# Optimization experiments

Hardware: AMD Instinct MI355X
Metric: run time of the kernel (lower is better)

## Reference

```python
import jax, jax.numpy as jnp
import numpy as np

B, C, H, W = 8, 256, 64, 64
HEADS, PTS = 8, 4
HD = C // HEADS
CIN_G, CIN_S, COUT = 1024, 320, 320


def _sine_pe(c, h, w):
    # LoFTR-style 2D sinusoidal position encoding, returns [C,H,W]
    pe = np.zeros((c, h, w), dtype=np.float32)
    y = np.broadcast_to(np.arange(h, dtype=np.float32)[None, :, None], (1, h, w))
    x = np.broadcast_to(np.arange(w, dtype=np.float32)[None, None, :], (1, h, w))
    div = np.exp(np.arange(0, c // 2, 2, dtype=np.float32) * (-np.log(10000.0) / (c // 2)))[:, None, None]
    pe[0::4] = np.sin(x * div)
    pe[1::4] = np.cos(x * div)
    pe[2::4] = np.sin(y * div)
    pe[3::4] = np.cos(y * div)
    return jnp.asarray(pe)


def _ref_points(h, w):
    # faithful to source: meshgrid over (W,H) 'ij', stack (col,row), flatten w-major
    rows = np.linspace(0, 1, w, dtype=np.float32)
    cols = np.linspace(0, 1, h, dtype=np.float32)
    R, Cg = np.meshgrid(rows, cols, indexing='ij')  # [W,H]
    return jnp.asarray(np.stack([Cg, R], -1).reshape(-1, 2))  # [W*H,2]


PE = _sine_pe(C, H, W)
RP = _ref_points(H, W)


def conv1x1(x, w, b):
    return jnp.einsum('bchw,oc->bohw', x, w) + b[None, :, None, None]


def deform_attn(qf, vf, vp_w, vp_b, so_w, so_b, aw_w, aw_b, op_w, op_b):
    # qf: [B,Nq,C]  vf: [B,Nv,C]  (single level, H x W value map)
    Bn, Nq, Cc = qf.shape
    v = (vf @ vp_w + vp_b).reshape(Bn, -1, HEADS, HD).transpose(0, 2, 1, 3)  # [B,h,Nv,hd]
    off = (qf @ so_w + so_b).reshape(Bn, Nq, HEADS, PTS, 2)
    aw = jax.nn.softmax((qf @ aw_w + aw_b).reshape(Bn, Nq, HEADS, PTS), axis=-1)
    loc = RP[None, :, None, None, :] + off / jnp.array([W, H], qf.dtype)  # [B,Nq,h,P,2]
    # grid_sample align_corners=False, zero padding
    px = loc[..., 0] * W - 0.5
    py = loc[..., 1] * H - 0.5
    x0 = jnp.floor(px).astype(jnp.int32)
    y0 = jnp.floor(py).astype(jnp.int32)
    wx = px - x0
    wy = py - y0
    out = jnp.zeros((Bn, HEADS, Nq, PTS, HD), qf.dtype)
    for dx, dy, wgt in ((0, 0, (1 - wx) * (1 - wy)), (1, 0, wx * (1 - wy)),
                        (0, 1, (1 - wx) * wy), (1, 1, wx * wy)):
        xi = x0 + dx
        yi = y0 + dy
        valid = ((xi >= 0) & (xi < W) & (yi >= 0) & (yi < H)).astype(qf.dtype)
        idx = jnp.clip(yi, 0, H - 1) * W + jnp.clip(xi, 0, W - 1)  # [B,Nq,h,P]
        idx_h = idx.transpose(0, 2, 1, 3).reshape(Bn, HEADS, Nq * PTS)
        g = jnp.take_along_axis(v, idx_h[..., None], axis=2).reshape(Bn, HEADS, Nq, PTS, HD)
        out = out + g * (wgt * valid).transpose(0, 2, 1, 3)[..., None]
    o = (out * aw.transpose(0, 2, 1, 3)[..., None]).sum(3)  # [B,h,Nq,hd]
    o = o.transpose(0, 2, 1, 3).reshape(Bn, Nq, Cc)
    return o @ op_w + op_b + qf  # mmcv: output_proj + identity (dropout=eval)


def cross_attn(q, value, vp_w, vp_b, so_w, so_b, aw_w, aw_b, op_w, op_b):
    qp = q + PE[None]  # query += pe
    qf = qp.reshape(qp.shape[0], C, H * W).transpose(0, 2, 1)
    vf = value.reshape(value.shape[0], C, H * W).transpose(0, 2, 1)
    o = deform_attn(qf, vf, vp_w, vp_b, so_w, so_b, aw_w, aw_b, op_w, op_b)
    o = o.transpose(0, 2, 1).reshape(qp.shape)
    return o + qp


def setup_inputs() -> dict:
    key = jax.random.key(0)
    ks = jax.random.split(key, 40)
    inp = {}
    inp['ground'] = jax.random.normal(ks[0], (B, CIN_G, H, W), jnp.float32)
    inp['sat'] = jax.random.normal(ks[1], (B, CIN_S, H, W), jnp.float32)
    inp['osm'] = jax.random.normal(ks[2], (B, CIN_S, H, W), jnp.float32)
    i = [3]
    def p(name, shape, scale=0.02):
        inp[name] = jax.random.normal(ks[i[0]], shape, jnp.float32) * scale
        i[0] += 1
    p('gc_w', (C, CIN_G)); p('gc_b', (C,))
    p('sc_w', (C, CIN_S)); p('sc_b', (C,))
    p('up_w', (COUT, C)); p('up_b', (COUT,))
    p('a_w1', (C, 64)); p('a_b1', (64,))
    p('a_w2', (64, 1)); p('a_b2', (1,))
    for pre in ('sat_', 'osm_'):
        p(pre + 'vp_w', (C, C)); p(pre + 'vp_b', (C,))
        p(pre + 'so_w', (C, HEADS * PTS * 2)); p(pre + 'so_b', (HEADS * PTS * 2,))
        p(pre + 'aw_w', (C, HEADS * PTS)); p(pre + 'aw_b', (HEADS * PTS,))
        p(pre + 'op_w', (C, C)); p(pre + 'op_b', (C,))
    inp['index'] = 0
    return inp


def reference(ground, sat, osm, gc_w, gc_b, sc_w, sc_b, up_w, up_b,
              a_w1, a_b1, a_w2, a_b2,
              sat_vp_w, sat_vp_b, sat_so_w, sat_so_b, sat_aw_w, sat_aw_b, sat_op_w, sat_op_b,
              osm_vp_w, osm_vp_b, osm_so_w, osm_so_b, osm_aw_w, osm_aw_b, osm_op_w, osm_op_b,
              index):
    del index  # params for index=0 already selected
    g = conv1x1(ground, gc_w, gc_b)
    s = conv1x1(sat, sc_w, sc_b)
    o = conv1x1(osm, sc_w, sc_b)  # source bug: osm projected with sat_convs
    gf = g.reshape(B, C, H * W).transpose(0, 2, 1)
    alpha = jax.nn.sigmoid(jax.nn.relu(gf @ a_w1 + a_b1) @ a_w2 + a_b2)  # [B,Nq,1]
    a = alpha.mean(axis=1)[:, :, None, None]  # [B,1,1,1]
    sat_out = cross_attn(g, s, sat_vp_w, sat_vp_b, sat_so_w, sat_so_b, sat_aw_w, sat_aw_b, sat_op_w, sat_op_b)
    # torch in-place `query += pe` inside ca_sat mutates `ground`, so ca_osm sees g + PE
    osm_out = cross_attn(g + PE[None], o, osm_vp_w, osm_vp_b, osm_so_w, osm_so_b, osm_aw_w, osm_aw_b, osm_op_w, osm_op_b)
    fused = a * sat_out + (1.0 - a) * osm_out
    return conv1x1(fused, up_w, up_b), a
```

## Files before the change

kernel.cpp:

```cpp
#include <hip/hip_runtime.h>
#include <cstddef>
#include <cstdint>

#define NB 8
#define NQ 4096

typedef __attribute__((ext_vector_type(8))) short bfrag8;
typedef __attribute__((ext_vector_type(4))) float facc4;
typedef __attribute__((ext_vector_type(4))) unsigned short us4;
typedef __attribute__((ext_vector_type(8))) unsigned short us8;

__device__ __forceinline__ float bf2f(unsigned short u) {
  union { unsigned int i; float f; } v; v.i = ((unsigned int)u) << 16; return v.f;
}
__device__ __forceinline__ unsigned short f2bf(float f) {
  union { float f; unsigned int i; } v; v.f = f;
  unsigned int r = v.i + 0x7FFFu + ((v.i >> 16) & 1u);
  return (unsigned short)(r >> 16);
}
__device__ __forceinline__ void gload16(const void* g, void* l) {
  __builtin_amdgcn_global_load_lds(
      (const __attribute__((address_space(1))) void*)g,
      (__attribute__((address_space(3))) void*)l, 16, 0, 0);
}

struct PrepArgs {
  const float *gc_w, *up_w, *up_b;
  const float *so_w0, *so_b0, *so_w1, *so_b1;
  const float *aw_w0, *aw_b0, *aw_w1, *aw_b1;
  const float *a_w1;
  const float *op_w0, *op_w1;
  unsigned short *PET, *WG, *WUP, *OPT0, *OPT1, *SOWS;
  float *BUPP, *SOBS;
};

__global__ __launch_bounds__(256) void mega_prep(PrepArgs p) {
  const int blk = blockIdx.x, t = threadIdx.x;
  if (blk < 4096) {
    int idx = blk * 256 + t;
    int q = idx >> 8, c = idx & 255;
    int h = q >> 6, w = q & 63;
    int k = c >> 2, m = c & 3;
    float dv = expf((float)(2 * k) * (-9.210340371976184f / 128.0f));
    float arg = ((m < 2) ? (float)w : (float)h) * dv;
    p.PET[idx] = f2bf(((m & 1) == 0) ? sinf(arg) : cosf(arg));
  } else if (blk < 5120) {
    int i = (blk - 4096) * 256 + t;
    p.WG[i] = f2bf(p.gc_w[i]);
  } else if (blk < 5504) {
    int i = (blk - 5120) * 256 + t;
    int m = i >> 8, k = i & 255;
    p.WUP[i] = (m < 320) ? f2bf(p.up_w[m * 256 + k]) : 0;
  } else if (blk < 5505) {
    p.BUPP[t] = (t < 320) ? p.up_b[t] : 0.f;
    if (t < 128) {
      int i2 = 256 + t;
      p.BUPP[i2] = (i2 < 320) ? p.up_b[i2] : 0.f;
    }
  } else if (blk < 6017) {
    int i = (blk - 5505) * 256 + t;
    int which = i >> 16, j = i & 65535;
    int o = j >> 8, k = j & 255;
    (which ? p.OPT1 : p.OPT0)[j] = f2bf((which ? p.op_w1 : p.op_w0)[k * 256 + o]);
  } else {
    int i = (blk - 6017) * 256 + t;
    int row = i >> 8, k = i & 255;
    float v = 0.f;
    if (row < 256) {
      int br = row >> 7, rr = row & 127;
      const float* sw = br ? p.so_w1 : p.so_w0;
      const float* aw = br ? p.aw_w1 : p.aw_w0;
      if (rr < 64) v = sw[k * 64 + rr];
      else if (rr < 96) v = aw[k * 32 + (rr - 64)];
    } else if (row < 320) {
      v = p.a_w1[k * 64 + (row - 256)];
    }
    p.SOWS[i] = f2bf(v);
    if (i < 256) {
      int br = i >> 7, rr = i & 127;
      const float* sb = br ? p.so_b1 : p.so_b0;
      const float* ab = br ? p.aw_b1 : p.aw_b0;
      p.SOBS[i] = (rr < 64) ? sb[rr] : ((rr < 96) ? ab[rr - 64] : 0.f);
    }
  }
}

__global__ __launch_bounds__(256) void k_wv(const float* __restrict__ vp_w0,
                                            const float* __restrict__ vp_b0,
                                            const float* __restrict__ vp_w1,
                                            const float* __restrict__ vp_b1,
                                            const float* __restrict__ sc_w,
                                            const float* __restrict__ sc_b,
                                            unsigned short* __restrict__ WV0,
                                            unsigned short* __restrict__ WV1,
                                            float* __restrict__ BV0,
                                            float* __restrict__ BV1) {
  const int br = blockIdx.y, kt = blockIdx.x, k0 = kt * 20, t = threadIdx.x;
  const float* vp = br ? vp_w1 : vp_w0;
  unsigned short* WV = br ? WV1 : WV0;
  __shared__ float vt[32][256];
  __shared__ float st[32][20];
  __shared__ float sb[32];
  float acc[20] = {};
  float accB = 0.f;
  for (int c0 = 0; c0 < 256; c0 += 32) {
    __syncthreads();
#pragma unroll
    for (int cc = 0; cc < 32; ++cc)
      vt[cc][t] = vp[(size_t)(c0 + cc) * 256 + t];
    for (int i = t; i < 640; i += 256)
      st[i / 20][i % 20] = sc_w[(size_t)(c0 + i / 20) * 320 + k0 + (i % 20)];
    if (t < 32) sb[t] = sc_b[c0 + t];
    __syncthreads();
#pragma unroll
    for (int cc = 0; cc < 32; ++cc) {
      float v = vt[cc][t];
      accB = fmaf(v, sb[cc], accB);
#pragma unroll
      for (int j = 0; j < 20; ++j)
        acc[j] = fmaf(v, st[cc][j], acc[j]);
    }
  }
#pragma unroll
  for (int j = 0; j < 20; ++j) WV[(size_t)t * 320 + k0 + j] = f2bf(acc[j]);
  if (kt == 0) (br ? BV1 : BV0)[t] = (br ? vp_b1 : vp_b0)[t] + accB;
}

struct GArgs {
  const unsigned short* W[2];
  const unsigned short* X[2];
  const float* bias[2];
  void* out[2];
  float rscale[2];
  int K, ldm, bmask, brshift;
};
template <int MODE>
__global__ __launch_bounds__(256) void gemm_bf16(GArgs g) {
  __shared__ unsigned short As[8192];
  __shared__ unsigned short Bs[8192];
  const int t = threadIdx.x;
  const int lane = t & 63, w = t >> 6;
  const int z = blockIdx.z;
  const int b = z & g.bmask, br = z >> g.brshift;
  const int K = g.K;
  const int n0 = blockIdx.x * 128;
  const unsigned short* W = g.W[br];
  const unsigned short* Xb = g.X[br] + (size_t)b * NQ * K;

  const unsigned short* asrc[4];
  const unsigned short* bsrc[4];
  unsigned short* adst[4];
  unsigned short* bdst[4];
#pragma unroll
  for (int i = 0; i < 4; ++i) {
    int cid = i * 256 + t;
    int row = cid >> 3;
    int cc = (cid & 7) ^ (row & 7);
    asrc[i] = W + (size_t)row * K + cc * 8;
    bsrc[i] = Xb + (size_t)(n0 + row) * K + cc * 8;
    adst[i] = &As[i * 2048 + w * 512];
    bdst[i] = &Bs[i * 2048 + w * 512];
  }
  const int wm = (w >> 1) * 64, wn = (w & 1) * 64;
  const int l15 = lane & 15, l4 = lane >> 4;
  facc4 acc[4][4];
#pragma unroll
  for (int i = 0; i < 4; ++i)
#pragma unroll
    for (int j = 0; j < 4; ++j) acc[i][j] = facc4{0.f, 0.f, 0.f, 0.f};

  for (int k0 = 0; k0 < K; k0 += 64) {
    if (k0) __syncthreads();
#pragma unroll
    for (int i = 0; i < 4; ++i) {
      gload16(asrc[i], adst[i]);
      gload16(bsrc[i], bdst[i]);
      asrc[i] += 64; bsrc[i] += 64;
    }
    __syncthreads();
#pragma unroll
    for (int kk = 0; kk < 2; ++kk) {
      bfrag8 af[4], bf[4];
#pragma unroll
      for (int mi = 0; mi < 4; ++mi) {
        int row = wm + mi * 16 + l15;
        af[mi] = *reinterpret_cast<const bfrag8*>(&As[row * 64 + (((kk * 4 + l4) ^ (row & 7)) * 8)]);
      }
#pragma unroll
      for (int ni = 0; ni < 4; ++ni) {
        int row = wn + ni * 16 + l15;
        bf[ni] = *reinterpret_cast<const bfrag8*>(&Bs[row * 64 + (((kk * 4 + l4) ^ (row & 7)) * 8)]);
      }
#pragma unroll
      for (int mi = 0; mi < 4; ++mi)
#pragma unroll
        for (int ni = 0; ni < 4; ++ni)
          acc[mi][ni] = __builtin_amdgcn_mfma_f32_16x16x32_bf16(af[mi], bf[ni], acc[mi][ni], 0, 0, 0);
    }
  }
  const size_t bq = (size_t)b * NQ;
#pragma unroll
  for (int mi = 0; mi < 4; ++mi) {
#pragma unroll
    for (int ni = 0; ni < 4; ++ni) {
      int m = wm + mi * 16 + l4 * 4;
      int n = n0 + wn + ni * 16 + l15;
      facc4 v = acc[mi][ni];
      unsigned short* o16 = (unsigned short*)g.out[br];
      float sc = g.rscale[br];
      float4 bv = *reinterpret_cast<const float4*>(&g.bias[br][m]);
      us4 pk;
      pk[0] = f2bf(v[0] * sc + bv.x); pk[1] = f2bf(v[1] * sc + bv.y);
      pk[2] = f2bf(v[2] * sc + bv.z); pk[3] = f2bf(v[3] * sc + bv.w);
      *reinterpret_cast<us4*>(&o16[(bq + n) * g.ldm + m]) = pk;
    }
  }
}

struct NArgs {
  const unsigned short* W[2];
  const void* X[2];
  const float* bias[2];
  void* out[2];
  const unsigned short* G;
  const unsigned short* PET;
  const float* afin;
  float rs[2];
  int K, zmask, zshift;
};
template <int BSRC, int MODE>
__global__ __launch_bounds__(256) void gemm_n64(NArgs g) {
  __shared__ unsigned short As[16384];
  __shared__ unsigned short Bs[4096];
  const int t = threadIdx.x;
  const int lane = t & 63, w = t >> 6;
  const int z = blockIdx.z;
  const int b = z & g.zmask, br = z >> g.zshift;
  const int K = g.K;
  const int n0 = blockIdx.x * 64;

  const unsigned short* W = g.W[br];
  const unsigned short* asrc[8];
  unsigned short* adst[8];
#pragma unroll
  for (int i = 0; i < 8; ++i) {
    int c = t + 256 * i;
    int row = c >> 3;
    int k8 = (c & 7) ^ (row & 7);
    asrc[i] = W + (size_t)row * K + k8 * 8;
    adst[i] = &As[w * 512 + i * 2048];
  }

  const unsigned short* bsrc16[2];
  unsigned short* bdst16[2];
  const float* bsrcf = nullptr;
  const int kb = t >> 4, nb = t & 15;
  if constexpr (BSRC == 0) {
    const unsigned short* Xh = (const unsigned short*)g.X[br];
#pragma unroll
    for (int i = 0; i < 2; ++i) {
      int c = t + 256 * i;
      int n = c >> 3;
      int k8 = (c & 7) ^ (n & 7);
      bsrc16[i] = Xh + ((size_t)b * NQ + n0 + n) * K + k8 * 8;
      bdst16[i] = &Bs[w * 512 + i * 2048];
    }
  } else {
    const float* Xf = (const float*)g.X[br];
    bsrcf = Xf + (size_t)b * K * NQ + (size_t)(kb * 4) * NQ + n0 + nb * 4;
  }

  const int l15 = lane & 15, l4 = lane >> 4;
  facc4 acc[4][4];
#pragma unroll
  for (int i = 0; i < 4; ++i)
#pragma unroll
    for (int j = 0; j < 4; ++j) acc[i][j] = facc4{0.f, 0.f, 0.f, 0.f};

  for (int k0 = 0; k0 < K; k0 += 64) {
    if (k0) __syncthreads();
#pragma unroll
    for (int i = 0; i < 8; ++i) {
      gload16(asrc[i], adst[i]);
      asrc[i] += 64;
    }
    if constexpr (BSRC == 0) {
      gload16(bsrc16[0], bdst16[0]); bsrc16[0] += 64;
      gload16(bsrc16[1], bdst16[1]); bsrc16[1] += 64;
    } else {
      float vv[4][4];
#pragma unroll
      for (int r = 0; r < 4; ++r) {
        float4 v = *reinterpret_cast<const float4*>(bsrcf + (size_t)k0 * NQ + (size_t)r * NQ);
        vv[r][0] = v.x; vv[r][1] = v.y; vv[r][2] = v.z; vv[r][3] = v.w;
      }
#pragma unroll
      for (int c = 0; c < 4; ++c) {
        int n = nb * 4 + c;
        us4 pk;
        pk[0] = f2bf(vv[0][c]); pk[1] = f2bf(vv[1][c]);
        pk[2] = f2bf(vv[2][c]); pk[3] = f2bf(vv[3][c]);
        int off = n * 64 + (((kb >> 1) ^ (n & 7)) * 8) + (kb & 1) * 4;
        *reinterpret_cast<us4*>(&Bs[off]) = pk;
      }
    }
    __syncthreads();
#pragma unroll
    for (int kk = 0; kk < 2; ++kk) {
      bfrag8 af[4], bf[4];
#pragma unroll
      for (int mi = 0; mi < 4; ++mi) {
        int row = w * 64 + mi * 16 + l15;
        af[mi] = *reinterpret_cast<const bfrag8*>(&As[row * 64 + (((kk * 4 + l4) ^ (row & 7)) * 8)]);
      }
#pragma unroll
      for (int ni = 0; ni < 4; ++ni) {
        int row = ni * 16 + l15;
        bf[ni] = *reinterpret_cast<const bfrag8*>(&Bs[row * 64 + (((kk * 4 + l4) ^ (row & 7)) * 8)]);
      }
#pragma unroll
      for (int mi = 0; mi < 4; ++mi)
#pragma unroll
        for (int ni = 0; ni < 4; ++ni)
          acc[mi][ni] = __builtin_amdgcn_mfma_f32_16x16x32_bf16(af[mi], bf[ni], acc[mi][ni], 0, 0, 0);
    }
  }

  const size_t bq = (size_t)b * NQ;
  unsigned short* o16 = (unsigned short*)g.out[br];
#pragma unroll
  for (int mi = 0; mi < 4; ++mi) {
#pragma unroll
    for (int ni = 0; ni < 4; ++ni) {
      int m = w * 64 + mi * 16 + l4 * 4;
      int n = n0 + ni * 16 + l15;
      facc4 v = acc[mi][ni];
      float4 bv = *reinterpret_cast<const float4*>(&g.bias[br][m]);
      float rv[4] = {v[0] + bv.x, v[1] + bv.y, v[2] + bv.z, v[3] + bv.w};
      if constexpr (MODE == 6) {
        float a = g.afin[b];
        float s = br ? (1.f - a) : a;
        float rsc = g.rs[br];
        us4 gv = *reinterpret_cast<const us4*>(&g.G[(bq + n) * 256 + m]);
        us4 pv = *reinterpret_cast<const us4*>(&g.PET[(size_t)n * 256 + m]);
#pragma unroll
        for (int r = 0; r < 4; ++r)
          rv[r] = s * (rv[r] + 2.f * bf2f(gv[r]) + rsc * bf2f(pv[r]));
      }
      us4 pk;
#pragma unroll
      for (int r = 0; r < 4; ++r) pk[r] = f2bf(rv[r]);
      *reinterpret_cast<us4*>(&o16[(bq + n) * 256 + m]) = pk;
    }
  }
}

struct SAArgs {
  const unsigned short *W;
  const unsigned short *G;
  const unsigned short *PESOS;
  const float *b1, *w2, *b2;
  unsigned short *SWS;
  float *partial;
};
__global__ __launch_bounds__(384) void k_swalpha(SAArgs g) {
  __shared__ unsigned short As[24576];
  __shared__ unsigned short Bs[4096];
  const int t = threadIdx.x;
  const int lane = t & 63, w = t >> 6;
  const int b = blockIdx.z;
  const int n0 = blockIdx.x * 64;

  const unsigned short* asrc[8];
  unsigned short* adst[8];
#pragma unroll
  for (int i = 0; i < 8; ++i) {
    int c = t + 384 * i;
    int row = c >> 3;
    int k8 = (c & 7) ^ (row & 7);
    asrc[i] = g.W + (size_t)row * 256 + k8 * 8;
    adst[i] = &As[w * 512 + i * 3072];
  }
  const bool bst = t < 256;
  const unsigned short* bsrc[2];
// ... 60 lines not shown
        int m = w * 64 + mi * 16 + l4 * 4;
        int n = n0 + ni * 16 + l15;
        facc4 v = acc[mi][ni];
        us4 rr = *reinterpret_cast<const us4*>(&g.PESOS[(size_t)n * 256 + m]);
        us4 pk;
#pragma unroll
        for (int r = 0; r < 4; ++r) pk[r] = f2bf(v[r] + bf2f(rr[r]));
        *reinterpret_cast<us4*>(&g.SWS[(bq + n) * 256 + m]) = pk;
      }
    }
  } else if (w == 4) {
    float b2v = g.b2[0];
    float ssum = 0.f;
#pragma unroll
    for (int ni = 0; ni < 4; ++ni) {
      float s = 0.f;
#pragma unroll
      for (int mi = 0; mi < 4; ++mi) {
#pragma unroll
        for (int r = 0; r < 4; ++r) {
          int hid = mi * 16 + l4 * 4 + r;
          s += fmaxf(acc[mi][ni][r] + g.b1[hid], 0.f) * g.w2[hid];
        }
      }
      s += __shfl_xor(s, 16);
      s += __shfl_xor(s, 32);
      ssum += 1.f / (1.f + expf(-(s + b2v)));
    }
    ssum += __shfl_xor(ssum, 1);
    ssum += __shfl_xor(ssum, 2);
    ssum += __shfl_xor(ssum, 4);
    ssum += __shfl_xor(ssum, 8);
    if (lane == 0) g.partial[b * 64 + blockIdx.x] = ssum;
  }
}

__global__ __launch_bounds__(64) void k_alpha_fin(const float* __restrict__ partial,
                                                  float* __restrict__ afin,
                                                  float* __restrict__ out_a) {
  int b = blockIdx.x;
  float s = partial[b * 64 + threadIdx.x];
#pragma unroll
  for (int off = 32; off; off >>= 1) s += __shfl_xor(s, off);
  if (threadIdx.x == 0) {
    float a = s * (1.f / 4096.f);
    afin[b] = a;
    out_a[b] = a;
  }
}

__global__ __launch_bounds__(384) void gemm_up(const unsigned short* __restrict__ W,
                                               const unsigned short* __restrict__ S0,
                                               const unsigned short* __restrict__ S1,
                                               const float* __restrict__ bias,
                                               float* __restrict__ out) {
  __shared__ unsigned short As[24576];
  __shared__ unsigned short Bs[4096];
  const int t = threadIdx.x;
  const int lane = t & 63, w = t >> 6;
  const int b = blockIdx.z;
  const int n0 = blockIdx.x * 64;

  const unsigned short* asrc[8];
  unsigned short* adst[8];
#pragma unroll
  for (int i = 0; i < 8; ++i) {
    int c = t + 384 * i;
    int row = c >> 3;
    int k8 = (c & 7) ^ (row & 7);
    asrc[i] = W + (size_t)row * 256 + k8 * 8;
    adst[i] = &As[w * 512 + i * 3072];
  }
  const bool bst = t < 256;
  size_t bidx[2];
  if (bst) {
#pragma unroll
    for (int i = 0; i < 2; ++i) {
      int c = t + 256 * i;
      int n = c >> 3;
      int bk8 = (c & 7) ^ (n & 7);
      bidx[i] = ((size_t)b * NQ + n0 + n) * 256 + bk8 * 8;
    }
  }

  const int l15 = lane & 15, l4 = lane >> 4;
  facc4 acc[4][4];
#pragma unroll
  for (int i = 0; i < 4; ++i)
#pragma unroll
    for (int j = 0; j < 4; ++j) acc[i][j] = facc4{0.f, 0.f, 0.f, 0.f};

  for (int k0 = 0; k0 < 256; k0 += 64) {
    if (k0) __syncthreads();
#pragma unroll
    for (int i = 0; i < 8; ++i) {
      gload16(asrc[i], adst[i]);
      asrc[i] += 64;
    }
    if (bst) {
#pragma unroll
      for (int i = 0; i < 2; ++i) {
        us8 x = *reinterpret_cast<const us8*>(&S0[bidx[i] + k0]);
        us8 y = *reinterpret_cast<const us8*>(&S1[bidx[i] + k0]);
        us8 o;
#pragma unroll
        for (int j = 0; j < 8; ++j) o[j] = f2bf(bf2f(x[j]) + bf2f(y[j]));
        *reinterpret_cast<us8*>(&Bs[(t + 256 * i) * 8]) = o;
      }
    }
    __syncthreads();
#pragma unroll
    for (int kk = 0; kk < 2; ++kk) {
      bfrag8 af[4], bf[4];
#pragma unroll
      for (int mi = 0; mi < 4; ++mi) {
        int row = w * 64 + mi * 16 + l15;
        af[mi] = *reinterpret_cast<const bfrag8*>(&As[row * 64 + (((kk * 4 + l4) ^ (row & 7)) * 8)]);
      }
#pragma unroll
      for (int ni = 0; ni < 4; ++ni) {
        int row = ni * 16 + l15;
        bf[ni] = *reinterpret_cast<const bfrag8*>(&Bs[row * 64 + (((kk * 4 + l4) ^ (row & 7)) * 8)]);
      }
#pragma unroll
      for (int mi = 0; mi < 4; ++mi)
#pragma unroll
        for (int ni = 0; ni < 4; ++ni)
          acc[mi][ni] = __builtin_amdgcn_mfma_f32_16x16x32_bf16(af[mi], bf[ni], acc[mi][ni], 0, 0, 0);
    }
  }
#pragma unroll
  for (int mi = 0; mi < 4; ++mi) {
    int m = w * 64 + mi * 16 + l4 * 4;
    if (m >= 320) continue;
#pragma unroll
    for (int ni = 0; ni < 4; ++ni) {
      int n = n0 + ni * 16 + l15;
      facc4 v = acc[mi][ni];
#pragma unroll
      for (int r = 0; r < 4; ++r)
        out[((size_t)b * 320 + m + r) * NQ + n] = v[r] + bias[m + r];
    }
  }
}

__global__ __launch_bounds__(256) void k_sample(const unsigned short* __restrict__ VP0,
                                                const unsigned short* __restrict__ VP1,
                                                const unsigned short* __restrict__ SWS,
                                                unsigned short* __restrict__ OATT0,
                                                unsigned short* __restrict__ OATT1) {
  int y = blockIdx.y;
  int b = y & 7, br = y >> 3;
  int q0 = blockIdx.x * 8;
  const unsigned short* VP = (br ? VP1 : VP0) + (size_t)b * NQ * 256;
  const unsigned short* SWp = SWS + ((size_t)b * NQ + q0) * 256 + br * 128;
  unsigned short* OATT = (br ? OATT1 : OATT0) + ((size_t)b * NQ + q0) * 256;
  __shared__ unsigned short sws[1024];
  int t = threadIdx.x;
  {
    int row = t >> 5, col = (t & 31) * 4;
    *reinterpret_cast<us4*>(&sws[row * 128 + col]) =
        *reinterpret_cast<const us4*>(&SWp[(size_t)row * 256 + col]);
  }
  __syncthreads();
  int qi = t >> 5, ss = t & 31, head = ss >> 2, hdg = ss & 3;
  int q = q0 + qi;
  const unsigned short* sw = &sws[qi * 128];
  float l0 = bf2f(sw[64 + head * 4 + 0]);
  float l1 = bf2f(sw[64 + head * 4 + 1]);
  float l2 = bf2f(sw[64 + head * 4 + 2]);
  float l3 = bf2f(sw[64 + head * 4 + 3]);
  float mx = fmaxf(fmaxf(l0, l1), fmaxf(l2, l3));
  float e0 = expf(l0 - mx), e1 = expf(l1 - mx), e2 = expf(l2 - mx), e3 = expf(l3 - mx);
  float inv = 1.f / (e0 + e1 + e2 + e3);
  float aw[4] = {e0 * inv, e1 * inv, e2 * inv, e3 * inv};
  float rpx = (float)(q & 63) * (64.f / 63.f) - 0.5f;
  float rpy = (float)(q >> 6) * (64.f / 63.f) - 0.5f;
  const unsigned short* vb = VP + head * 32 + hdg * 8;
  float acc[8] = {};
#pragma unroll
  for (int p = 0; p < 4; ++p) {
    float px = rpx + bf2f(sw[head * 8 + p * 2 + 0]);
    float py = rpy + bf2f(sw[head * 8 + p * 2 + 1]);
    float fx = floorf(px), fy = floorf(py);
    int x0 = (int)fx, y0 = (int)fy;
    float wx = px - fx, wy = py - fy;
#pragma unroll
    for (int dy = 0; dy < 2; ++dy) {
#pragma unroll
      for (int dx = 0; dx < 2; ++dx) {
        int xi = x0 + dx, yi = y0 + dy;
        if (xi >= 0 && xi < 64 && yi >= 0 && yi < 64) {
          float wa = aw[p] * (dx ? wx : 1.f - wx) * (dy ? wy : 1.f - wy);
          bfrag8 v = *reinterpret_cast<const bfrag8*>(&vb[(size_t)(yi * 64 + xi) * 256]);
#pragma unroll
          for (int j = 0; j < 8; ++j) acc[j] = fmaf(wa, bf2f((unsigned short)v[j]), acc[j]);
        }
      }
    }
  }
  us8 o;
#pragma unroll
  for (int j = 0; j < 8; ++j) o[j] = f2bf(acc[j]);
  *reinterpret_cast<us8*>(&OATT[qi * 256 + ss * 8]) = o;
}

extern "C" void kernel_launch(void* const* d_in, const int* in_sizes, int n_in,
                              void* d_out, int out_size, void* d_ws, size_t ws_size,
                              hipStream_t stream) {
  const float* ground = (const float*)d_in[0];
  const float* sat = (const float*)d_in[1];
  const float* osm = (const float*)d_in[2];
  const float* gc_w = (const float*)d_in[3];
  const float* gc_b = (const float*)d_in[4];
  const float* sc_w = (const float*)d_in[5];
  const float* sc_b = (const float*)d_in[6];
  const float* up_w = (const float*)d_in[7];
  const float* up_b = (const float*)d_in[8];
  const float* a_w1 = (const float*)d_in[9];
  const float* a_b1 = (const float*)d_in[10];
  const float* a_w2 = (const float*)d_in[11];
  const float* a_b2 = (const float*)d_in[12];
  const float* vp_w[2] = {(const float*)d_in[13], (const float*)d_in[21]};
  const float* vp_b[2] = {(const float*)d_in[14], (const float*)d_in[22]};
  const float* so_w[2] = {(const float*)d_in[15], (const float*)d_in[23]};
  const float* so_b[2] = {(const float*)d_in[16], (const float*)d_in[24]};
  const float* aw_w[2] = {(const float*)d_in[17], (const float*)d_in[25]};
  const float* aw_b[2] = {(const float*)d_in[18], (const float*)d_in[26]};
  const float* op_w[2] = {(const float*)d_in[19], (const float*)d_in[27]};
  const float* op_b[2] = {(const float*)d_in[20], (const float*)d_in[28]};

  char* wsb = (char*)d_ws;
  const size_t MBy = 1 << 20;
  unsigned short* PET  = (unsigned short*)(wsb);
  unsigned short* WG   = (unsigned short*)(wsb + 2 * MBy);
  unsigned short* WV0  = (unsigned short*)(wsb + 2 * MBy + 524288);
  unsigned short* WV1  = (unsigned short*)(wsb + 2 * MBy + 786432);
  unsigned short* WUP  = (unsigned short*)(wsb + 3 * MBy);
  unsigned short* OPT0 = (unsigned short*)(wsb + 3 * MBy + 262144);
  unsigned short* OPT1 = (unsigned short*)(wsb + 3 * MBy + 393216);
  unsigned short* SOWS = (unsigned short*)(wsb + 3 * MBy + 524288);
  unsigned short* PESOS = (unsigned short*)(wsb + 4 * MBy);
  float* SOBS = (float*)(wsb + 6 * MBy);
  float* BV0  = (float*)(wsb + 6 * MBy + 4096);
  float* BV1  = (float*)(wsb + 6 * MBy + 8192);
  float* BUPP = (float*)(wsb + 6 * MBy + 12288);
  float* PART = (float*)(wsb + 6 * MBy + 16384);
  float* AFIN = (float*)(wsb + 6 * MBy + 32768);
  unsigned short* G     = (unsigned short*)(wsb + 8 * MBy);
  unsigned short* VP0b  = (unsigned short*)(wsb + 24 * MBy);
  unsigned short* VP1b  = (unsigned short*)(wsb + 40 * MBy);
  unsigned short* SWS   = (unsigned short*)(wsb + 56 * MBy);
  unsigned short* OATT0 = (unsigned short*)(wsb + 72 * MBy);
  unsigned short* OATT1 = (unsigned short*)(wsb + 88 * MBy);
  unsigned short* SATO  = (unsigned short*)(wsb + 104 * MBy);
  unsigned short* OSMO  = (unsigned short*)(wsb + 120 * MBy);

  float* out32 = (float*)d_out;
  float* out_a = out32 + (size_t)NB * 320 * NQ;

  dim3 blk(256);

  {
    PrepArgs p;
    p.gc_w = gc_w; p.up_w = up_w; p.up_b = up_b;
    p.so_w0 = so_w[0]; p.so_b0 = so_b[0]; p.so_w1 = so_w[1]; p.so_b1 = so_b[1];
    p.aw_w0 = aw_w[0]; p.aw_b0 = aw_b[0]; p.aw_w1 = aw_w[1]; p.aw_b1 = aw_b[1];
    p.a_w1 = a_w1;
    p.op_w0 = op_w[0]; p.op_w1 = op_w[1];
    p.PET = PET; p.WG = WG; p.WUP = WUP;
    p.OPT0 = OPT0; p.OPT1 = OPT1; p.SOWS = SOWS;
    p.BUPP = BUPP; p.SOBS = SOBS;
    mega_prep<<<dim3(6401), blk, 0, stream>>>(p);
  }
  k_wv<<<dim3(16, 2), blk, 0, stream>>>(vp_w[0], vp_b[0], vp_w[1], vp_b[1],
                                        sc_w, sc_b, WV0, WV1, BV0, BV1);

  {
    GArgs a = {};
    a.W[0] = SOWS; a.W[1] = SOWS + 128 * 256;
    a.X[0] = PET;  a.X[1] = PET;
    a.bias[0] = SOBS; a.bias[1] = SOBS + 128;
    a.out[0] = PESOS; a.out[1] = PESOS + 128;
    a.rscale[0] = 1.f; a.rscale[1] = 2.f;
    a.K = 256; a.ldm = 256; a.bmask = 0; a.brshift = 0;
    gemm_bf16<1><<<dim3(32, 1, 2), blk, 0, stream>>>(a);
  }

  {
    NArgs a = {};
    a.W[0] = WG; a.W[1] = WG;
    a.X[0] = ground; a.X[1] = ground;
    a.bias[0] = gc_b; a.bias[1] = gc_b;
    a.out[0] = G; a.out[1] = G;
    a.K = 1024; a.zmask = 7; a.zshift = 31;
    gemm_n64<1, 0><<<dim3(64, 1, NB), blk, 0, stream>>>(a);
  }

  {
    SAArgs a;
    a.W = SOWS; a.G = G; a.PESOS = PESOS;
    a.b1 = a_b1; a.w2 = a_w2; a.b2 = a_b2;
    a.SWS = SWS; a.partial = PART;
    k_swalpha<<<dim3(64, 1, NB), dim3(384), 0, stream>>>(a);
  }
  k_alpha_fin<<<dim3(NB), dim3(64), 0, stream>>>(PART, AFIN, out_a);

  {
    NArgs a = {};
    a.W[0] = WV0; a.W[1] = WV1;
    a.X[0] = sat; a.X[1] = osm;
    a.bias[0] = BV0; a.bias[1] = BV1;
    a.out[0] = VP0b; a.out[1] = VP1b;
    a.K = 320; a.zmask = 7; a.zshift = 3;
    gemm_n64<1, 0><<<dim3(64, 1, 16), blk, 0, stream>>>(a);
  }

  k_sample<<<dim3(512, 16), blk, 0, stream>>>(VP0b, VP1b, SWS, OATT0, OATT1);

  {
    NArgs a = {};
    a.W[0] = OPT0; a.W[1] = OPT1;
    a.X[0] = OATT0; a.X[1] = OATT1;
    a.bias[0] = op_b[0]; a.bias[1] = op_b[1];
    a.out[0] = SATO; a.out[1] = OSMO;
    a.G = G; a.PET = PET; a.afin = AFIN;
    a.rs[0] = 2.f; a.rs[1] = 4.f;
    a.K = 256; a.zmask = 7; a.zshift = 3;
    gemm_n64<0, 6><<<dim3(64, 1, 16), blk, 0, stream>>>(a);
  }

  gemm_up<<<dim3(64, 1, NB), dim3(384), 0, stream>>>(WUP, SATO, OSMO, BUPP, out32);
}
```

Baseline: 272.1 us.

## Fuse output projections with upsample GEMM and merge projection launches

Moves the value-weight folding kernel into the prep kernel. Merges the ground conv, the two value projections and the PE offset GEMM into one multi-route GEMM launch. Fuses the alpha finalize, both output projections, the blend and the upsample conv into one kernel that keeps the blended tile in LDS. This removes several launches and the round trip of the SATO/OSMO intermediates through global memory. In exchange the fused kernel uses a large LDS footprint, which may lower occupancy, and runs its two projection passes serially within each block.

```diff
diff --git a/kernel.cpp b/kernel.cpp
--- a/kernel.cpp
+++ b/kernel.cpp
@@ -30,11 +30,15 @@
   const float *aw_w0, *aw_b0, *aw_w1, *aw_b1;
   const float *a_w1;
   const float *op_w0, *op_w1;
-  unsigned short *PET, *WG, *WUP, *OPT0, *OPT1, *SOWS;
-  float *BUPP, *SOBS;
+  const float *vp_w0, *vp_b0, *vp_w1, *vp_b1, *sc_w, *sc_b;
+  unsigned short *PET, *WG, *WUP, *OPT0, *OPT1, *SOWS, *WV0, *WV1;
+  float *BUPP, *SOBS, *BV0, *BV1;
 };
 
 __global__ __launch_bounds__(256) void mega_prep(PrepArgs p) {
+  __shared__ float vt[32][256];
+  __shared__ float st[32][20];
+  __shared__ float sb[32];
   const int blk = blockIdx.x, t = threadIdx.x;
   if (blk < 4096) {
     int idx = blk * 256 + t;
@@ -62,7 +66,7 @@
     int which = i >> 16, j = i & 65535;
     int o = j >> 8, k = j & 255;
     (which ? p.OPT1 : p.OPT0)[j] = f2bf((which ? p.op_w1 : p.op_w0)[k * 256 + o]);
-  } else {
+  } else if (blk < 6401) {
     int i = (blk - 6017) * 256 + t;
     int row = i >> 8, k = i & 255;
     float v = 0.f;
@@ -78,168 +82,63 @@
     p.SOWS[i] = f2bf(v);
     if (i < 256) {
       int br = i >> 7, rr = i & 127;
-      const float* sb = br ? p.so_b1 : p.so_b0;
-      const float* ab = br ? p.aw_b1 : p.aw_b0;
-      p.SOBS[i] = (rr < 64) ? sb[rr] : ((rr < 96) ? ab[rr - 64] : 0.f);
-    }
-  }
-}
-
-__global__ __launch_bounds__(256) void k_wv(const float* __restrict__ vp_w0,
-                                            const float* __restrict__ vp_b0,
-                                            const float* __restrict__ vp_w1,
-                                            const float* __restrict__ vp_b1,
-                                            const float* __restrict__ sc_w,
-                                            const float* __restrict__ sc_b,
-                                            unsigned short* __restrict__ WV0,
-                                            unsigned short* __restrict__ WV1,
-                                            float* __restrict__ BV0,
-                                            float* __restrict__ BV1) {
-  const int br = blockIdx.y, kt = blockIdx.x, k0 = kt * 20, t = threadIdx.x;
-  const float* vp = br ? vp_w1 : vp_w0;
-  unsigned short* WV = br ? WV1 : WV0;
-  __shared__ float vt[32][256];
-  __shared__ float st[32][20];
-  __shared__ float sb[32];
-  float acc[20] = {};
-  float accB = 0.f;
-  for (int c0 = 0; c0 < 256; c0 += 32) {
-    __syncthreads();
-#pragma unroll
-    for (int cc = 0; cc < 32; ++cc)
-      vt[cc][t] = vp[(size_t)(c0 + cc) * 256 + t];
-    for (int i = t; i < 640; i += 256)
-      st[i / 20][i % 20] = sc_w[(size_t)(c0 + i / 20) * 320 + k0 + (i % 20)];
-    if (t < 32) sb[t] = sc_b[c0 + t];
-    __syncthreads();
-#pragma unroll
-    for (int cc = 0; cc < 32; ++cc) {
-      float v = vt[cc][t];
-      accB = fmaf(v, sb[cc], accB);
-#pragma unroll
-      for (int j = 0; j < 20; ++j)
-        acc[j] = fmaf(v, st[cc][j], acc[j]);
-    }
-  }
-#pragma unroll
-  for (int j = 0; j < 20; ++j) WV[(size_t)t * 320 + k0 + j] = f2bf(acc[j]);
-  if (kt == 0) (br ? BV1 : BV0)[t] = (br ? vp_b1 : vp_b0)[t] + accB;
-}
-
-struct GArgs {
-  const unsigned short* W[2];
-  const unsigned short* X[2];
-  const float* bias[2];
-  void* out[2];
-  float rscale[2];
-  int K, ldm, bmask, brshift;
+      const float* sbp = br ? p.so_b1 : p.so_b0;
+      const float* abp = br ? p.aw_b1 : p.aw_b0;
+      p.SOBS[i] = (rr < 64) ? sbp[rr] : ((rr < 96) ? abp[rr - 64] : 0.f);
+    }
+  } else {
+    int bi = blk - 6401;
+    int kt = bi & 15, br = bi >> 4, k0 = kt * 20;
+    const float* vp = br ? p.vp_w1 : p.vp_w0;
+    unsigned short* WV = br ? p.WV1 : p.WV0;
+    float acc[20] = {};
+    float accB = 0.f;
+    for (int c0 = 0; c0 < 256; c0 += 32) {
+      __syncthreads();
+#pragma unroll
+      for (int cc = 0; cc < 32; ++cc)
+        vt[cc][t] = vp[(size_t)(c0 + cc) * 256 + t];
+      for (int i = t; i < 640; i += 256)
+        st[i / 20][i % 20] = p.sc_w[(size_t)(c0 + i / 20) * 320 + k0 + (i % 20)];
+      if (t < 32) sb[t] = p.sc_b[c0 + t];
+      __syncthreads();
+#pragma unroll
+      for (int cc = 0; cc < 32; ++cc) {
+        float v = vt[cc][t];
+        accB = fmaf(v, sb[cc], accB);
+#pragma unroll
+        for (int j = 0; j < 20; ++j)
+          acc[j] = fmaf(v, st[cc][j], acc[j]);
+      }
+    }
+#pragma unroll
+    for (int j = 0; j < 20; ++j) WV[(size_t)t * 320 + k0 + j] = f2bf(acc[j]);
+    if (kt == 0) (br ? p.BV1 : p.BV0)[t] = (br ? p.vp_b1 : p.vp_b0)[t] + accB;
+  }
+}
+
+struct MArgs {
+  const unsigned short* W[4];
+  const void* X[4];
+  const float* bias[4];
+  void* out[4];
+  int K[4];
 };
-template <int MODE>
-__global__ __launch_bounds__(256) void gemm_bf16(GArgs g) {
-  __shared__ unsigned short As[8192];
-  __shared__ unsigned short Bs[8192];
-  const int t = threadIdx.x;
-  const int lane = t & 63, w = t >> 6;
-  const int z = blockIdx.z;
-  const int b = z & g.bmask, br = z >> g.brshift;
-  const int K = g.K;
-  const int n0 = blockIdx.x * 128;
-  const unsigned short* W = g.W[br];
-  const unsigned short* Xb = g.X[br] + (size_t)b * NQ * K;
-
-  const unsigned short* asrc[4];
-  const unsigned short* bsrc[4];
-  unsigned short* adst[4];
-  unsigned short* bdst[4];
-#pragma unroll
-  for (int i = 0; i < 4; ++i) {
-    int cid = i * 256 + t;
-    int row = cid >> 3;
-    int cc = (cid & 7) ^ (row & 7);
-    asrc[i] = W + (size_t)row * K + cc * 8;
-    bsrc[i] = Xb + (size_t)(n0 + row) * K + cc * 8;
-    adst[i] = &As[i * 2048 + w * 512];
-    bdst[i] = &Bs[i * 2048 + w * 512];
-  }
-  const int wm = (w >> 1) * 64, wn = (w & 1) * 64;
-  const int l15 = lane & 15, l4 = lane >> 4;
-  facc4 acc[4][4];
-#pragma unroll
-  for (int i = 0; i < 4; ++i)
-#pragma unroll
-    for (int j = 0; j < 4; ++j) acc[i][j] = facc4{0.f, 0.f, 0.f, 0.f};
-
-  for (int k0 = 0; k0 < K; k0 += 64) {
-    if (k0) __syncthreads();
-#pragma unroll
-    for (int i = 0; i < 4; ++i) {
-      gload16(asrc[i], adst[i]);
-      gload16(bsrc[i], bdst[i]);
-      asrc[i] += 64; bsrc[i] += 64;
-    }
-    __syncthreads();
-#pragma unroll
-    for (int kk = 0; kk < 2; ++kk) {
-      bfrag8 af[4], bf[4];
-#pragma unroll
-      for (int mi = 0; mi < 4; ++mi) {
-        int row = wm + mi * 16 + l15;
-        af[mi] = *reinterpret_cast<const bfrag8*>(&As[row * 64 + (((kk * 4 + l4) ^ (row & 7)) * 8)]);
-      }
-#pragma unroll
-      for (int ni = 0; ni < 4; ++ni) {
-        int row = wn + ni * 16 + l15;
-        bf[ni] = *reinterpret_cast<const bfrag8*>(&Bs[row * 64 + (((kk * 4 + l4) ^ (row & 7)) * 8)]);
-      }
-#pragma unroll
-      for (int mi = 0; mi < 4; ++mi)
-#pragma unroll
-        for (int ni = 0; ni < 4; ++ni)
-          acc[mi][ni] = __builtin_amdgcn_mfma_f32_16x16x32_bf16(af[mi], bf[ni], acc[mi][ni], 0, 0, 0);
-    }
-  }
-  const size_t bq = (size_t)b * NQ;
-#pragma unroll
-  for (int mi = 0; mi < 4; ++mi) {
-#pragma unroll
-    for (int ni = 0; ni < 4; ++ni) {
-      int m = wm + mi * 16 + l4 * 4;
-      int n = n0 + wn + ni * 16 + l15;
-      facc4 v = acc[mi][ni];
-      unsigned short* o16 = (unsigned short*)g.out[br];
-      float sc = g.rscale[br];
-      float4 bv = *reinterpret_cast<const float4*>(&g.bias[br][m]);
-      us4 pk;
-      pk[0] = f2bf(v[0] * sc + bv.x); pk[1] = f2bf(v[1] * sc + bv.y);
-      pk[2] = f2bf(v[2] * sc + bv.z); pk[3] = f2bf(v[3] * sc + bv.w);
-      *reinterpret_cast<us4*>(&o16[(bq + n) * g.ldm + m]) = pk;
-    }
-  }
-}
-
-struct NArgs {
-  const unsigned short* W[2];
-  const void* X[2];
-  const float* bias[2];
-  void* out[2];
-  const unsigned short* G;
-  const unsigned short* PET;
-  const float* afin;
-  float rs[2];
-  int K, zmask, zshift;
-};
-template <int BSRC, int MODE>
-__global__ __launch_bounds__(256) void gemm_n64(NArgs g) {
+__global__ __launch_bounds__(256) void gemm_mega(MArgs g) {
   __shared__ unsigned short As[16384];
   __shared__ unsigned short Bs[4096];
   const int t = threadIdx.x;
   const int lane = t & 63, w = t >> 6;
   const int z = blockIdx.z;
-  const int b = z & g.zmask, br = z >> g.zshift;
-  const int K = g.K;
+  int route, b;
+  if (z < 8) { route = 0; b = z; }
+  else if (z < 16) { route = 1; b = z - 8; }
+  else if (z < 24) { route = 2; b = z - 16; }
+  else { route = 3; b = 0; }
+  const int K = g.K[route];
   const int n0 = blockIdx.x * 64;
 
-  const unsigned short* W = g.W[br];
+  const unsigned short* W = g.W[route];
   const unsigned short* asrc[8];
   unsigned short* adst[8];
 #pragma unroll
@@ -255,18 +154,18 @@
   unsigned short* bdst16[2];
   const float* bsrcf = nullptr;
   const int kb = t >> 4, nb = t & 15;
-  if constexpr (BSRC == 0) {
-    const unsigned short* Xh = (const unsigned short*)g.X[br];
+  if (route == 3) {
+    const unsigned short* Xh = (const unsigned short*)g.X[3];
 #pragma unroll
     for (int i = 0; i < 2; ++i) {
       int c = t + 256 * i;
       int n = c >> 3;
       int k8 = (c & 7) ^ (n & 7);
-      bsrc16[i] = Xh + ((size_t)b * NQ + n0 + n) * K + k8 * 8;
+      bsrc16[i] = Xh + (size_t)(n0 + n) * K + k8 * 8;
       bdst16[i] = &Bs[w * 512 + i * 2048];
     }
   } else {
-    const float* Xf = (const float*)g.X[br];
+    const float* Xf = (const float*)g.X[route];
     bsrcf = Xf + (size_t)b * K * NQ + (size_t)(kb * 4) * NQ + n0 + nb * 4;
   }
 
@@ -284,7 +183,7 @@
       gload16(asrc[i], adst[i]);
       asrc[i] += 64;
     }
-    if constexpr (BSRC == 0) {
+    if (route == 3) {
       gload16(bsrc16[0], bdst16[0]); bsrc16[0] += 64;
       gload16(bsrc16[1], bdst16[1]); bsrc16[1] += 64;
     } else {
@@ -327,7 +226,8 @@
   }
 
   const size_t bq = (size_t)b * NQ;
-  unsigned short* o16 = (unsigned short*)g.out[br];
+  unsigned short* o16 = (unsigned short*)g.out[route];
+  const float* bias = g.bias[route];
 #pragma unroll
   for (int mi = 0; mi < 4; ++mi) {
 #pragma unroll
@@ -335,21 +235,11 @@
       int m = w * 64 + mi * 16 + l4 * 4;
       int n = n0 + ni * 16 + l15;
       facc4 v = acc[mi][ni];
-      float4 bv = *reinterpret_cast<const float4*>(&g.bias[br][m]);
-      float rv[4] = {v[0] + bv.x, v[1] + bv.y, v[2] + bv.z, v[3] + bv.w};
-      if constexpr (MODE == 6) {
-        float a = g.afin[b];
-        float s = br ? (1.f - a) : a;
-        float rsc = g.rs[br];
-        us4 gv = *reinterpret_cast<const us4*>(&g.G[(bq + n) * 256 + m]);
-        us4 pv = *reinterpret_cast<const us4*>(&g.PET[(size_t)n * 256 + m]);
-#pragma unroll
-        for (int r = 0; r < 4; ++r)
-          rv[r] = s * (rv[r] + 2.f * bf2f(gv[r]) + rsc * bf2f(pv[r]));
-      }
+      float sc = (route == 3 && m >= 128) ? 2.f : 1.f;
+      float4 bv = *reinterpret_cast<const float4*>(&bias[m]);
       us4 pk;
-#pragma unroll
-      for (int r = 0; r < 4; ++r) pk[r] = f2bf(rv[r]);
+      pk[0] = f2bf(v[0] * sc + bv.x); pk[1] = f2bf(v[1] * sc + bv.y);
+      pk[2] = f2bf(v[2] * sc + bv.z); pk[3] = f2bf(v[3] * sc + bv.w);
       *reinterpret_cast<us4*>(&o16[(bq + n) * 256 + m]) = pk;
     }
   }
@@ -476,115 +366,6 @@
     ssum += __shfl_xor(ssum, 4);
     ssum += __shfl_xor(ssum, 8);
     if (lane == 0) g.partial[b * 64 + blockIdx.x] = ssum;
-  }
-}
-
-__global__ __launch_bounds__(64) void k_alpha_fin(const float* __restrict__ partial,
-                                                  float* __restrict__ afin,
-                                                  float* __restrict__ out_a) {
-  int b = blockIdx.x;
-  float s = partial[b * 64 + threadIdx.x];
-#pragma unroll
-  for (int off = 32; off; off >>= 1) s += __shfl_xor(s, off);
-  if (threadIdx.x == 0) {
-    float a = s * (1.f / 4096.f);
-    afin[b] = a;
-    out_a[b] = a;
-  }
-}
-
-__global__ __launch_bounds__(384) void gemm_up(const unsigned short* __restrict__ W,
-                                               const unsigned short* __restrict__ S0,
-                                               const unsigned short* __restrict__ S1,
-                                               const float* __restrict__ bias,
-                                               float* __restrict__ out) {
-  __shared__ unsigned short As[24576];
-  __shared__ unsigned short Bs[4096];
-  const int t = threadIdx.x;
-  const int lane = t & 63, w = t >> 6;
-  const int b = blockIdx.z;
-  const int n0 = blockIdx.x * 64;
-
-  const unsigned short* asrc[8];
-  unsigned short* adst[8];
-#pragma unroll
-  for (int i = 0; i < 8; ++i) {
-    int c = t + 384 * i;
-    int row = c >> 3;
-    int k8 = (c & 7) ^ (row & 7);
-    asrc[i] = W + (size_t)row * 256 + k8 * 8;
-    adst[i] = &As[w * 512 + i * 3072];
-  }
-  const bool bst = t < 256;
-  size_t bidx[2];
-  if (bst) {
-#pragma unroll
-    for (int i = 0; i < 2; ++i) {
-      int c = t + 256 * i;
-      int n = c >> 3;
-      int bk8 = (c & 7) ^ (n & 7);
-      bidx[i] = ((size_t)b * NQ + n0 + n) * 256 + bk8 * 8;
-    }
-  }
-
-  const int l15 = lane & 15, l4 = lane >> 4;
-  facc4 acc[4][4];
-#pragma unroll
-  for (int i = 0; i < 4; ++i)
-#pragma unroll
-    for (int j = 0; j < 4; ++j) acc[i][j] = facc4{0.f, 0.f, 0.f, 0.f};
-
-  for (int k0 = 0; k0 < 256; k0 += 64) {
-    if (k0) __syncthreads();
-#pragma unroll
-    for (int i = 0; i < 8; ++i) {
-      gload16(asrc[i], adst[i]);
-      asrc[i] += 64;
-    }
-    if (bst) {
-#pragma unroll
-      for (int i = 0; i < 2; ++i) {
-        us8 x = *reinterpret_cast<const us8*>(&S0[bidx[i] + k0]);
-        us8 y = *reinterpret_cast<const us8*>(&S1[bidx[i] + k0]);
-        us8 o;
-#pragma unroll
-        for (int j = 0; j < 8; ++j) o[j] = f2bf(bf2f(x[j]) + bf2f(y[j]));
-        *reinterpret_cast<us8*>(&Bs[(t + 256 * i) * 8]) = o;
-      }
-    }
-    __syncthreads();
-#pragma unroll
-    for (int kk = 0; kk < 2; ++kk) {
-      bfrag8 af[4], bf[4];
-#pragma unroll
-      for (int mi = 0; mi < 4; ++mi) {
-        int row = w * 64 + mi * 16 + l15;
-        af[mi] = *reinterpret_cast<const bfrag8*>(&As[row * 64 + (((kk * 4 + l4) ^ (row & 7)) * 8)]);
-      }
-#pragma unroll
-      for (int ni = 0; ni < 4; ++ni) {
-        int row = ni * 16 + l15;
-        bf[ni] = *reinterpret_cast<const bfrag8*>(&Bs[row * 64 + (((kk * 4 + l4) ^ (row & 7)) * 8)]);
-      }
-#pragma unroll
-      for (int mi = 0; mi < 4; ++mi)
-#pragma unroll
-        for (int ni = 0; ni < 4; ++ni)
-          acc[mi][ni] = __builtin_amdgcn_mfma_f32_16x16x32_bf16(af[mi], bf[ni], acc[mi][ni], 0, 0, 0);
-    }
-  }
-#pragma unroll
-  for (int mi = 0; mi < 4; ++mi) {
-    int m = w * 64 + mi * 16 + l4 * 4;
-    if (m >= 320) continue;
-#pragma unroll
-    for (int ni = 0; ni < 4; ++ni) {
-      int n = n0 + ni * 16 + l15;
-      facc4 v = acc[mi][ni];
-#pragma unroll
-      for (int r = 0; r < 4; ++r)
-        out[((size_t)b * 320 + m + r) * NQ + n] = v[r] + bias[m + r];
-    }
   }
 }
 
@@ -647,6 +428,155 @@
 #pragma unroll
   for (int j = 0; j < 8; ++j) o[j] = f2bf(acc[j]);
   *reinterpret_cast<us8*>(&OATT[qi * 256 + ss * 8]) = o;
+}
+
+struct UArgs {
+  const unsigned short *OATT0, *OATT1, *OPT0, *OPT1, *G, *PET, *WUP;
+  const float *opb0, *opb1, *BUPP, *PART;
+  float *out, *out_a;
+};
+__global__ __launch_bounds__(256) void k_opup(UArgs g) {
+  __shared__ unsigned short As[20480];
+  __shared__ unsigned short Bs[4096];
+  __shared__ unsigned short P[16384];
+  const int t = threadIdx.x;
+  const int lane = t & 63, w = t >> 6;
+  const int b = blockIdx.y;
+  const int n0 = blockIdx.x * 64;
+  const int l15 = lane & 15, l4 = lane >> 4;
+  const size_t bq = (size_t)b * NQ;
+
+  float av = g.PART[b * 64 + lane];
+#pragma unroll
+  for (int off = 1; off < 64; off <<= 1) av += __shfl_xor(av, off);
+  const float a = av * (1.f / 4096.f);
+  if (blockIdx.x == 0 && t == 0) g.out_a[b] = a;
+
+  for (int br = 0; br < 2; ++br) {
+    const unsigned short* OPT = br ? g.OPT1 : g.OPT0;
+    const unsigned short* OATT = (br ? g.OATT1 : g.OATT0) + bq * 256;
+    const float* opb = br ? g.opb1 : g.opb0;
+    facc4 acc[4][4];
+#pragma unroll
+    for (int i = 0; i < 4; ++i)
+#pragma unroll
+      for (int j = 0; j < 4; ++j) acc[i][j] = facc4{0.f, 0.f, 0.f, 0.f};
+
+    for (int kt = 0; kt < 4; ++kt) {
+      __syncthreads();
+#pragma unroll
+      for (int i = 0; i < 8; ++i) {
+        int c = t + 256 * i;
+        int row = c >> 3;
+        int k8 = (c & 7) ^ (row & 7);
+        gload16(OPT + (size_t)row * 256 + kt * 64 + k8 * 8, &As[w * 512 + i * 2048]);
+      }
+#pragma unroll
+      for (int i = 0; i < 2; ++i) {
+        int c = t + 256 * i;
+        int n = c >> 3;
+        int k8 = (c & 7) ^ (n & 7);
+        gload16(OATT + (size_t)(n0 + n) * 256 + kt * 64 + k8 * 8, &Bs[w * 512 + i * 2048]);
+      }
+      __syncthreads();
+#pragma unroll
+      for (int kk = 0; kk < 2; ++kk) {
+        bfrag8 af[4], bf[4];
+#pragma unroll
+        for (int mi = 0; mi < 4; ++mi) {
+          int row = w * 64 + mi * 16 + l15;
+          af[mi] = *reinterpret_cast<const bfrag8*>(&As[row * 64 + (((kk * 4 + l4) ^ (row & 7)) * 8)]);
+        }
+#pragma unroll
+        for (int ni = 0; ni < 4; ++ni) {
+          int row = ni * 16 + l15;
+          bf[ni] = *reinterpret_cast<const bfrag8*>(&Bs[row * 64 + (((kk * 4 + l4) ^ (row & 7)) * 8)]);
+        }
+#pragma unroll
+        for (int mi = 0; mi < 4; ++mi)
+#pragma unroll
+          for (int ni = 0; ni < 4; ++ni)
+            acc[mi][ni] = __builtin_amdgcn_mfma_f32_16x16x32_bf16(af[mi], bf[ni], acc[mi][ni], 0, 0, 0);
+      }
+    }
+    const float rs = br ? 4.f : 2.f;
+    const float s = br ? (1.f - a) : a;
+#pragma unroll
+    for (int mi = 0; mi < 4; ++mi) {
+#pragma unroll
+      for (int ni = 0; ni < 4; ++ni) {
+        int m = w * 64 + mi * 16 + l4 * 4;
+        int nloc = ni * 16 + l15;
+        int n = n0 + nloc;
+        float4 bv = *reinterpret_cast<const float4*>(&opb[m]);
+        us4 gv = *reinterpret_cast<const us4*>(&g.G[(bq + n) * 256 + m]);
+        us4 pv = *reinterpret_cast<const us4*>(&g.PET[(size_t)n * 256 + m]);
+        facc4 v = acc[mi][ni];
+        float bb[4] = {bv.x, bv.y, bv.z, bv.w};
+        int pidx = nloc * 256 + (m >> 6) * 64 + ((((m >> 3) & 7) ^ (nloc & 7)) * 8) + (m & 7);
+        us4 pk;
+        if (br == 0) {
+#pragma unroll
+          for (int r = 0; r < 4; ++r)
+            pk[r] = f2bf(s * (v[r] + bb[r] + 2.f * bf2f(gv[r]) + rs * bf2f(pv[r])));
+        } else {
+          us4 old = *reinterpret_cast<const us4*>(&P[pidx]);
+#pragma unroll
+          for (int r = 0; r < 4; ++r)
+            pk[r] = f2bf(bf2f(old[r]) + s * (v[r] + bb[r] + 2.f * bf2f(gv[r]) + rs * bf2f(pv[r])));
+        }
+        *reinterpret_cast<us4*>(&P[pidx]) = pk;
+      }
+    }
+  }
+  __syncthreads();
+
+  facc4 au[5][4];
+#pragma unroll
+  for (int i = 0; i < 5; ++i)
+#pragma unroll
+    for (int j = 0; j < 4; ++j) au[i][j] = facc4{0.f, 0.f, 0.f, 0.f};
+
+  for (int kt = 0; kt < 4; ++kt) {
+    __syncthreads();
+#pragma unroll
+    for (int i = 0; i < 10; ++i) {
+      int c = t + 256 * i;
+      int row = c >> 3;
+      int k8 = (c & 7) ^ (row & 7);
+      gload16(g.WUP + (size_t)row * 256 + kt * 64 + k8 * 8, &As[w * 512 + i * 2048]);
+    }
+    __syncthreads();
+#pragma unroll
+    for (int kk = 0; kk < 2; ++kk) {
+      bfrag8 bf[4];
+#pragma unroll
+      for (int ni = 0; ni < 4; ++ni) {
+        int n = ni * 16 + l15;
+        bf[ni] = *reinterpret_cast<const bfrag8*>(&P[n * 256 + kt * 64 + (((kk * 4 + l4) ^ (n & 7)) * 8)]);
+      }
+#pragma unroll
+      for (int j = 0; j < 5; ++j) {
+        int row = (w * 5 + j) * 16 + l15;
+        bfrag8 af = *reinterpret_cast<const bfrag8*>(&As[row * 64 + (((kk * 4 + l4) ^ (row & 7)) * 8)]);
+#pragma unroll
+        for (int ni = 0; ni < 4; ++ni)
+          au[j][ni] = __builtin_amdgcn_mfma_f32_16x16x32_bf16(af, bf[ni], au[j][ni], 0, 0, 0);
+      }
+    }
+  }
+#pragma unroll
+  for (int j = 0; j < 5; ++j) {
+    int m = (w * 5 + j) * 16 + l4 * 4;
+#pragma unroll
+    for (int ni = 0; ni < 4; ++ni) {
+      int n = n0 + ni * 16 + l15;
+      facc4 v = au[j][ni];
+#pragma unroll
+      for (int r = 0; r < 4; ++r)
+        g.out[((size_t)b * 320 + m + r) * NQ + n] = v[r] + g.BUPP[m + r];
+    }
+  }
 }
 
 extern "C" void kernel_launch(void* const* d_in, const int* in_sizes, int n_in,
@@ -690,15 +620,12 @@
   float* BV1  = (float*)(wsb + 6 * MBy + 8192);
   float* BUPP = (float*)(wsb + 6 * MBy + 12288);
   float* PART = (float*)(wsb + 6 * MBy + 16384);
-  float* AFIN = (float*)(wsb + 6 * MBy + 32768);
   unsigned short* G     = (unsigned short*)(wsb + 8 * MBy);
   unsigned short* VP0b  = (unsigned short*)(wsb + 24 * MBy);
   unsigned short* VP1b  = (unsigned short*)(wsb + 40 * MBy);
   unsigned short* SWS   = (unsigned short*)(wsb + 56 * MBy);
   unsigned short* OATT0 = (unsigned short*)(wsb + 72 * MBy);
   unsigned short* OATT1 = (unsigned short*)(wsb + 88 * MBy);
-  unsigned short* SATO  = (unsigned short*)(wsb + 104 * MBy);
-  unsigned short* OSMO  = (unsigned short*)(wsb + 120 * MBy);
 
   float* out32 = (float*)d_out;
   float* out_a = out32 + (size_t)NB * 320 * NQ;
@@ -712,33 +639,21 @@
     p.aw_w0 = aw_w[0]; p.aw_b0 = aw_b[0]; p.aw_w1 = aw_w[1]; p.aw_b1 = aw_b[1];
     p.a_w1 = a_w1;
     p.op_w0 = op_w[0]; p.op_w1 = op_w[1];
+    p.vp_w0 = vp_w[0]; p.vp_b0 = vp_b[0]; p.vp_w1 = vp_w[1]; p.vp_b1 = vp_b[1];
+    p.sc_w = sc_w; p.sc_b = sc_b;
     p.PET = PET; p.WG = WG; p.WUP = WUP;
-    p.OPT0 = OPT0; p.OPT1 = OPT1; p.SOWS = SOWS;
-    p.BUPP = BUPP; p.SOBS = SOBS;
-    mega_prep<<<dim3(6401), blk, 0, stream>>>(p);
-  }
-  k_wv<<<dim3(16, 2), blk, 0, stream>>>(vp_w[0], vp_b[0], vp_w[1], vp_b[1],
-                                        sc_w, sc_b, WV0, WV1, BV0, BV1);
+    p.OPT0 = OPT0; p.OPT1 = OPT1; p.SOWS = SOWS; p.WV0 = WV0; p.WV1 = WV1;
+    p.BUPP = BUPP; p.SOBS = SOBS; p.BV0 = BV0; p.BV1 = BV1;
+    mega_prep<<<dim3(6433), blk, 0, stream>>>(p);
+  }
 
   {
-    GArgs a = {};
-    a.W[0] = SOWS; a.W[1] = SOWS + 128 * 256;
-    a.X[0] = PET;  a.X[1] = PET;
-    a.bias[0] = SOBS; a.bias[1] = SOBS + 128;
-    a.out[0] = PESOS; a.out[1] = PESOS + 128;
-    a.rscale[0] = 1.f; a.rscale[1] = 2.f;
-    a.K = 256; a.ldm = 256; a.bmask = 0; a.brshift = 0;
-    gemm_bf16<1><<<dim3(32, 1, 2), blk, 0, stream>>>(a);
-  }
-
-  {
-    NArgs a = {};
-    a.W[0] = WG; a.W[1] = WG;
-    a.X[0] = ground; a.X[1] = ground;
-    a.bias[0] = gc_b; a.bias[1] = gc_b;
-    a.out[0] = G; a.out[1] = G;
-    a.K = 1024; a.zmask = 7; a.zshift = 31;
-    gemm_n64<1, 0><<<dim3(64, 1, NB), blk, 0, stream>>>(a);
+    MArgs a;
+    a.W[0] = WG;    a.X[0] = ground; a.bias[0] = gc_b; a.out[0] = G;     a.K[0] = 1024;
+    a.W[1] = WV0;   a.X[1] = sat;    a.bias[1] = BV0;  a.out[1] = VP0b;  a.K[1] = 320;
+    a.W[2] = WV1;   a.X[2] = osm;    a.bias[2] = BV1;  a.out[2] = VP1b;  a.K[2] = 320;
+    a.W[3] = SOWS;  a.X[3] = PET;    a.bias[3] = SOBS; a.out[3] = PESOS; a.K[3] = 256;
+    gemm_mega<<<dim3(64, 1, 25), blk, 0, stream>>>(a);
   }
 
   {
@@ -748,31 +663,17 @@
     a.SWS = SWS; a.partial = PART;
     k_swalpha<<<dim3(64, 1, NB), dim3(384), 0, stream>>>(a);
   }
-  k_alpha_fin<<<dim3(NB), dim3(64), 0, stream>>>(PART, AFIN, out_a);
+
+  k_sample<<<dim3(512, 16), blk, 0, stream>>>(VP0b, VP1b, SWS, OATT0, OATT1);
 
   {
-    NArgs a = {};
-    a.W[0] = WV0; a.W[1] = WV1;
-    a.X[0] = sat; a.X[1] = osm;
-    a.bias[0] = BV0; a.bias[1] = BV1;
-    a.out[0] = VP0b; a.out[1] = VP1b;
-    a.K = 320; a.zmask = 7; a.zshift = 3;
-    gemm_n64<1, 0><<<dim3(64, 1, 16), blk, 0, stream>>>(a);
-  }
-
-  k_sample<<<dim3(512, 16), blk, 0, stream>>>(VP0b, VP1b, SWS, OATT0, OATT1);
-
-  {
-    NArgs a = {};
-    a.W[0] = OPT0; a.W[1] = OPT1;
-    a.X[0] = OATT0; a.X[1] = OATT1;
-    a.bias[0] = op_b[0]; a.bias[1] = op_b[1];
-    a.out[0] = SATO; a.out[1] = OSMO;
-    a.G = G; a.PET = PET; a.afin = AFIN;
-    a.rs[0] = 2.f; a.rs[1] = 4.f;
-    a.K = 256; a.zmask = 7; a.zshift = 3;
-    gemm_n64<0, 6><<<dim3(64, 1, 16), blk, 0, stream>>>(a);
-  }
-
-  gemm_up<<<dim3(64, 1, NB), dim3(384), 0, stream>>>(WUP, SATO, OSMO, BUPP, out32);
-}
+    UArgs a;
+    a.OATT0 = OATT0; a.OATT1 = OATT1;
+    a.OPT0 = OPT0; a.OPT1 = OPT1;
+    a.G = G; a.PET = PET; a.WUP = WUP;
+    a.opb0 = op_b[0]; a.opb1 = op_b[1];
+    a.BUPP = BUPP; a.PART = PART;
+    a.out = out32; a.out_a = out_a;
+    k_opup<<<dim3(64, NB), blk, 0, stream>>>(a);
+  }
+}
```

Result: faster. 244.2 us (-10.3%).
